# Kernel optimization log

Measured on AMD Instinct MI355X. Metric: run time of the kernel, lower is better.

Reference implementation:

```python
import jax, jax.numpy as jnp
import numpy as np

N_HEAD = 16

def setup_inputs() -> dict:
    key = jax.random.key(0)
    k1, k2, k3, k4, k5 = jax.random.split(key, 5)
    B, S, D = 2, 2048, 1024
    return {
        "hidden_states": jax.random.normal(k1, (B, S, D), jnp.float32),
        "w_attn": jax.random.normal(k2, (D, 3 * D), jnp.float32) * 0.02,
        "b_attn": jax.random.normal(k3, (3 * D,), jnp.float32) * 0.02,
        "w_proj": jax.random.normal(k4, (D, D), jnp.float32) * 0.02,
        "b_proj": jax.random.normal(k5, (D,), jnp.float32) * 0.02,
    }

def reference(hidden_states, w_attn, b_attn, w_proj, b_proj):
    B, S, D = hidden_states.shape
    H = N_HEAD
    Dh = D // H
    qkv = hidden_states @ w_attn + b_attn              # [B,S,3D]
    q, k, v = jnp.split(qkv, 3, axis=-1)
    def split_heads(x):
        return x.reshape(B, S, H, Dh).transpose(0, 2, 1, 3)  # [B,H,S,Dh]
    q, k, v = split_heads(q), split_heads(k), split_heads(v)
    # scale=True: divide by sqrt(head_dim) (v.size(-1))
    scores = jnp.einsum("bhqd,bhkd->bhqk", q, k) / jnp.sqrt(jnp.float32(Dh))
    attn = jax.nn.softmax(scores, axis=-1)             # [B,H,S,S]
    out = jnp.einsum("bhqk,bhkd->bhqd", attn, v)       # [B,H,S,Dh]
    out = out.transpose(0, 2, 1, 3).reshape(B, S, D)   # merge heads
    return out @ w_proj + b_proj
```

## Files before the change

kernel.cpp:

```cpp
#include <hip/hip_runtime.h>
#include <hip/hip_bf16.h>

typedef __attribute__((ext_vector_type(8))) short bf16x8;
typedef __attribute__((ext_vector_type(4))) float f32x4;
typedef __attribute__((ext_vector_type(16))) float f32x16;

#define LOG2E 1.4426950408889634f

__device__ inline unsigned short f2bf(float f) {
  union { float f; unsigned u; } x; x.f = f;
  unsigned u = x.u;
  unsigned r = u + 0x7FFFu + ((u >> 16) & 1u);
  return (unsigned short)(r >> 16);
}

__device__ inline unsigned cvtpk(float lo, float hi) {
  unsigned r;
  asm("v_cvt_pk_bf16_f32 %0, %1, %2" : "=v"(r) : "v"(lo), "v"(hi));
  return r;
}

__device__ inline void gload16(const unsigned short* g, unsigned short* l) {
  __builtin_amdgcn_global_load_lds(
      (const __attribute__((address_space(1))) unsigned int*)g,
      (__attribute__((address_space(3))) unsigned int*)l, 16, 0, 0);
}

template <int J>
__device__ inline bf16x8 pack_pfrag(f32x16 p) {
  int X, Y, Z, W;
  asm("v_cvt_pk_bf16_f32 %0, %1, %2" : "=v"(X) : "v"(p[J + 0]), "v"(p[J + 1]));
  asm("v_cvt_pk_bf16_f32 %0, %1, %2" : "=v"(Y) : "v"(p[J + 2]), "v"(p[J + 3]));
  asm("v_cvt_pk_bf16_f32 %0, %1, %2" : "=v"(Z) : "v"(p[J + 4]), "v"(p[J + 5]));
  asm("v_cvt_pk_bf16_f32 %0, %1, %2" : "=v"(W) : "v"(p[J + 6]), "v"(p[J + 7]));
  asm("v_permlane32_swap_b32 %0, %1" : "+v"(X), "+v"(Z));
  asm("v_permlane32_swap_b32 %0, %1" : "+v"(Y), "+v"(W));
  union { int w[4]; bf16x8 v; } u;
  u.w[0] = X; u.w[1] = Y; u.w[2] = Z; u.w[3] = W;
  return u.v;
}

__global__ __launch_bounds__(256) void cvt_bf16(const float* __restrict__ X,
                                                unsigned short* __restrict__ Y, int n4) {
  int i = blockIdx.x * blockDim.x + threadIdx.x;
  int stride = gridDim.x * blockDim.x;
  for (; i < n4; i += stride) {
    float4 v = reinterpret_cast<const float4*>(X)[i];
    ushort4 o;
    o.x = f2bf(v.x); o.y = f2bf(v.y); o.z = f2bf(v.z); o.w = f2bf(v.w);
    reinterpret_cast<ushort4*>(Y)[i] = o;
  }
}

__global__ __launch_bounds__(256) void transpose_cvt(const float* __restrict__ W,
                                                     unsigned short* __restrict__ WT,
                                                     int K, int N) {
  __shared__ unsigned short Tl[64][72];
  const int t = threadIdx.x;
  const int n0 = blockIdx.x * 64, k0 = blockIdx.y * 64;
#pragma unroll
  for (int i = 0; i < 4; ++i) {
    int idx = t + i * 256;
    int r = idx >> 4, c4 = (idx & 15) << 2;
    float4 v = *reinterpret_cast<const float4*>(&W[(size_t)(k0 + r) * N + n0 + c4]);
    Tl[c4 + 0][r] = f2bf(v.x);
    Tl[c4 + 1][r] = f2bf(v.y);
    Tl[c4 + 2][r] = f2bf(v.z);
    Tl[c4 + 3][r] = f2bf(v.w);
  }
  __syncthreads();
#pragma unroll
  for (int i = 0; i < 2; ++i) {
    int idx = t + i * 256;
    int rr = idx >> 3, cc = (idx & 7) << 3;
    *reinterpret_cast<int4*>(&WT[(size_t)(n0 + rr) * K + k0 + cc]) =
        *reinterpret_cast<const int4*>(&Tl[rr][cc]);
  }
}

#define GST(bs, kt)                                                             \
  {                                                                             \
    const unsigned short* Ap = Ab + (kt) * 32;                                  \
    const unsigned short* Bp = Bb + (kt) * 32;                                  \
    _Pragma("unroll") for (int i = 0; i < 2; ++i) {                             \
      int row = i * 64 + wid * 16 + s_r;                                        \
      gload16(&Ap[(size_t)row * 1024 + s_c], &Al[bs][i * 2048 + wid * 512]);    \
      gload16(&Bp[(size_t)row * 1024 + s_c], &Bl[bs][i * 2048 + wid * 512]);    \
    }                                                                           \
  }

#define GBODY(br)                                                               \
  {                                                                             \
    bf16x8 af[4], bfv[4];                                                       \
    _Pragma("unroll") for (int mm = 0; mm < 4; ++mm) {                          \
      int row = wr + mm * 16 + lr;                                              \
      af[mm] = *reinterpret_cast<const bf16x8*>(                                \
          &Al[br][row * 32 + ((kq ^ (lr & 3)) << 3)]);                          \
    }                                                                           \
    _Pragma("unroll") for (int nn = 0; nn < 4; ++nn) {                          \
      int row = wc + nn * 16 + lr;                                              \
      bfv[nn] = *reinterpret_cast<const bf16x8*>(                               \
          &Bl[br][row * 32 + ((kq ^ (lr & 3)) << 3)]);                          \
    }                                                                           \
    _Pragma("unroll") for (int mm = 0; mm < 4; ++mm)                            \
      _Pragma("unroll") for (int nn = 0; nn < 4; ++nn)                          \
        acc[mm][nn] =                                                           \
            __builtin_amdgcn_mfma_f32_16x16x32_bf16(af[mm], bfv[nn],            \
                                                    acc[mm][nn], 0, 0, 0);      \
  }

#define VMC4 asm volatile("s_waitcnt vmcnt(4)" ::: "memory");
#define VMC0 asm volatile("s_waitcnt vmcnt(0)" ::: "memory");
#define BAR __builtin_amdgcn_s_barrier();

__global__ __launch_bounds__(256) void gemm_qkv_b(
    const unsigned short* __restrict__ A, const unsigned short* __restrict__ Bt,
    const float* __restrict__ bias,
    unsigned short* __restrict__ qw, unsigned short* __restrict__ kw,
    unsigned short* __restrict__ vtg) {
  __shared__ unsigned short Al[3][4096];
  __shared__ unsigned short Bl[3][4096];
  const int t = threadIdx.x, lane = t & 63, wid = t >> 6;
  const int wr = (wid >> 1) * 64, wc = (wid & 1) * 64;
  const int orig = blockIdx.x + 24 * blockIdx.y;
  const int nid = (orig & 7) * 96 + (orig >> 3);
  const int row0 = (nid / 24) * 128, col0 = (nid % 24) * 128;
  const int lr = lane & 15, kq = lane >> 4;
  const int s_r = lane >> 2;
  const int s_c = ((lane & 3) ^ (s_r & 3)) * 8;
  const unsigned short* Ab = A + (size_t)row0 * 1024;
  const unsigned short* Bb = Bt + (size_t)col0 * 1024;
  f32x4 acc[4][4] = {};

  GST(0, 0) GST(1, 1)
  VMC4 BAR
  for (int tt = 0; tt < 30; tt += 3) {
    GST(2, tt + 2) GBODY(0) VMC4 BAR
    GST(0, tt + 3) GBODY(1) VMC4 BAR
    GST(1, tt + 4) GBODY(2) VMC4 BAR
  }
  GBODY(0) VMC0 BAR
  GBODY(1)

  const int rbase = (lane >> 4) * 4;
#pragma unroll
  for (int mm = 0; mm < 4; ++mm) {
#pragma unroll
    for (int nn = 0; nn < 4; ++nn) {
      int c = col0 + wc + nn * 16 + lr;
      int which = c >> 10;
      int d = c & 1023;
      int h = d >> 6, dh = d & 63;
      float bv = bias[c];
      int m0 = row0 + wr + mm * 16 + rbase;
      int b = m0 >> 11, s0 = m0 & 2047;
      if (which == 2) {
        int kt = s0 >> 6, key0 = s0 & 63;
        ushort4 pv;
        pv.x = f2bf(acc[mm][nn][0] + bv);
        pv.y = f2bf(acc[mm][nn][1] + bv);
        pv.z = f2bf(acc[mm][nn][2] + bv);
        pv.w = f2bf(acc[mm][nn][3] + bv);
        *reinterpret_cast<ushort4*>(
            &vtg[(((size_t)(b * 16 + h) * 32 + kt) * 64 + dh) * 64 + key0]) = pv;
      } else {
        unsigned short* dst = (which == 0) ? qw : kw;
#pragma unroll
        for (int r = 0; r < 4; ++r)
          dst[(((size_t)b * 16 + h) * 2048 + (s0 + r)) * 64 + dh] = f2bf(acc[mm][nn][r] + bv);
      }
    }
  }
}

__global__ __launch_bounds__(256) void gemm_proj_b(
    const unsigned short* __restrict__ A, const unsigned short* __restrict__ Bt,
    const float* __restrict__ bias, float* __restrict__ out) {
  const int N = 1024;
  __shared__ unsigned short Al[3][4096];
  __shared__ unsigned short Bl[3][4096];
  const int t = threadIdx.x, lane = t & 63, wid = t >> 6;
  const int wr = (wid >> 1) * 64, wc = (wid & 1) * 64;
  const int orig = blockIdx.x + 8 * blockIdx.y;
  const int nid = (orig & 7) * 32 + (orig >> 3);
  const int row0 = (nid >> 3) * 128, col0 = (nid & 7) * 128;
  const int lr = lane & 15, kq = lane >> 4;
  const int s_r = lane >> 2;
  const int s_c = ((lane & 3) ^ (s_r & 3)) * 8;
  const unsigned short* Ab = A + (size_t)row0 * 1024;
  const unsigned short* Bb = Bt + (size_t)col0 * 1024;
  f32x4 acc[4][4] = {};

  GST(0, 0) GST(1, 1)
  VMC4 BAR
  for (int tt = 0; tt < 30; tt += 3) {
    GST(2, tt + 2) GBODY(0) VMC4 BAR
    GST(0, tt + 3) GBODY(1) VMC4 BAR
    GST(1, tt + 4) GBODY(2) VMC4 BAR
  }
  GBODY(0) VMC0 BAR
  GBODY(1)

  const int rbase = (lane >> 4) * 4;
#pragma unroll
  for (int mm = 0; mm < 4; ++mm) {
#pragma unroll
    for (int nn = 0; nn < 4; ++nn) {
      int c = col0 + wc + nn * 16 + lr;
      float bv = bias[c];
#pragma unroll
      for (int r = 0; r < 4; ++r) {
        int m = row0 + wr + mm * 16 + rbase + r;
        out[(size_t)m * N + c] = acc[mm][nn][r] + bv;
      }
    }
  }
}

__global__ __launch_bounds__(512, 4) void attn_kernel(
    const unsigned short* __restrict__ qw, const unsigned short* __restrict__ kw,
    const unsigned short* __restrict__ vtg, unsigned short* __restrict__ ow) {
  __shared__ char smem[65536];
  unsigned short* KV = (unsigned short*)smem;
  unsigned short* Ol = (unsigned short*)smem;
  float* EX = (float*)(smem + 18432);
  const int t = threadIdx.x, lane = t & 63, wid = t >> 6;
  const int half = wid >> 2, wq = wid & 3;
  const int l31 = lane & 31, hi = lane >> 5;
  const int orig = blockIdx.x + 16 * blockIdx.y;
  const int nid = (orig & 7) * 64 + (orig >> 3);
  const int qt = nid & 15, bh = nid >> 4;
  const int b = bh >> 4, h = bh & 15;
  const unsigned short* Qg = qw + (size_t)bh * 2048 * 64;
  const unsigned short* Kg = kw + (size_t)bh * 2048 * 64;
  const unsigned short* Vg = vtg + (size_t)bh * 32 * 4096;
  const int q0 = qt * 128 + wq * 32;
  const float F = 0.125f * LOG2E;
  const float mF = 16.0f * F;

  union { short s[8]; bf16x8 v; } one_u;
#pragma unroll
  for (int i = 0; i < 8; ++i) one_u.s[i] = (short)0x3F80;
  const bf16x8 ones = one_u.v;

  bf16x8 qf[4];
#pragma unroll
  for (int kc = 0; kc < 4; ++kc)
    qf[kc] = *reinterpret_cast<const bf16x8*>(&Qg[(q0 + l31) * 64 + kc * 16 + hi * 8]);

  f32x16 oA = {0,0,0,0,0,0,0,0,0,0,0,0,0,0,0,0};
  f32x16 oB = {0,0,0,0,0,0,0,0,0,0,0,0,0,0,0,0};
  f32x16 lC = {0,0,0,0,0,0,0,0,0,0,0,0,0,0,0,0};

  const int srow_lo = lane >> 3;
  const int scg = (lane & 7) ^ srow_lo;

#define STAGE(buf, kt)                                                              \
  {                                                                                 \
    const unsigned short* Kt = Kg + (size_t)(kt) * 4096;                            \
    const unsigned short* Vs = Vg + (size_t)(kt) * 4096;                            \
    unsigned short* Kl = KV + half * 16384 + (buf) * 8192;                          \
    unsigned short* Vl = Kl + 4096;                                                 \
    _Pragma("unroll") for (int i = 0; i < 2; ++i) {                                 \
      int chunk = wq * 2 + i;                                                       \
      int row = chunk * 8 + srow_lo;                                                \
      gload16(&Kt[row * 64 + scg * 8], &Kl[chunk * 512]);                           \
      gload16(&Vs[row * 64 + scg * 8], &Vl[chunk * 512]);                           \
    }                                                                               \
  }

  const int kt0 = half * 16;
  STAGE(0, kt0)

  for (int it = 0; it < 16; ++it) {
    const int cur = it & 1;
    if (it + 1 < 16) {
      STAGE(cur ^ 1, kt0 + it + 1)
      asm volatile("s_waitcnt vmcnt(4)" ::: "memory");
    } else {
      asm volatile("s_waitcnt vmcnt(0)" ::: "memory");
    }
    __builtin_amdgcn_s_barrier();
    const unsigned short* Kl = KV + half * 16384 + cur * 8192;
    const unsigned short* Vl = Kl + 4096;

    f32x16 sA = {0,0,0,0,0,0,0,0,0,0,0,0,0,0,0,0};
    f32x16 sB = {0,0,0,0,0,0,0,0,0,0,0,0,0,0,0,0};
    __builtin_amdgcn_s_setprio(1);
#pragma unroll
    for (int kc = 0; kc < 4; ++kc) {
      bf16x8 k0f = *reinterpret_cast<const bf16x8*>(
          &Kl[l31 * 64 + (((kc * 2 + hi) ^ (l31 & 7)) << 3)]);
      bf16x8 k1f = *reinterpret_cast<const bf16x8*>(
          &Kl[(32 + l31) * 64 + (((kc * 2 + hi) ^ (l31 & 7)) << 3)]);
      sA = __builtin_amdgcn_mfma_f32_32x32x16_bf16(k0f, qf[kc], sA, 0, 0, 0);
      sB = __builtin_amdgcn_mfma_f32_32x32x16_bf16(k1f, qf[kc], sB, 0, 0, 0);
    }
    __builtin_amdgcn_s_setprio(0);

#pragma unroll
    for (int j = 0; j < 16; ++j) {
      sA[j] = exp2f(sA[j] * F - mF);
      sB[j] = exp2f(sB[j] * F - mF);
    }

    bf16x8 pf0 = pack_pfrag<0>(sA);
    bf16x8 pf1 = pack_pfrag<8>(sA);
    bf16x8 pf2 = pack_pfrag<0>(sB);
    bf16x8 pf3 = pack_pfrag<8>(sB);

    __builtin_amdgcn_s_setprio(1);
#pragma unroll
    for (int c = 0; c < 4; ++c) {
      bf16x8 pf = (c == 0) ? pf0 : (c == 1) ? pf1 : (c == 2) ? pf2 : pf3;
      int g = c * 2 + hi;
      bf16x8 v0f = *reinterpret_cast<const bf16x8*>(
          &Vl[l31 * 64 + ((g ^ (l31 & 7)) << 3)]);
      bf16x8 v1f = *reinterpret_cast<const bf16x8*>(
          &Vl[(32 + l31) * 64 + ((g ^ (l31 & 7)) << 3)]);
      oA = __builtin_amdgcn_mfma_f32_32x32x16_bf16(v0f, pf, oA, 0, 0, 0);
      oB = __builtin_amdgcn_mfma_f32_32x32x16_bf16(v1f, pf, oB, 0, 0, 0);
      lC = __builtin_amdgcn_mfma_f32_32x32x16_bf16(ones, pf, lC, 0, 0, 0);
    }
    __builtin_amdgcn_s_setprio(0);
    __builtin_amdgcn_s_barrier();
  }
#undef STAGE

  __syncthreads();
  if (half == 1) {
    float* e = EX + ((size_t)(wq * 64 + lane)) * 34;
#pragma unroll
    for (int j = 0; j < 16; ++j) { e[j] = oA[j]; e[16 + j] = oB[j]; }
    e[32] = lC[0];
  }
  __syncthreads();
  if (half == 0) {
    const float* e = EX + ((size_t)(wq * 64 + lane)) * 34;
    float linv = 1.0f / (lC[0] + e[32]);
    unsigned short* orow_l = Ol + (wq * 32 + l31) * 72;
#pragma unroll
    for (int g = 0; g < 4; ++g) {
      float a0 = (oA[4 * g + 0] + e[4 * g + 0]) * linv;
      float a1v = (oA[4 * g + 1] + e[4 * g + 1]) * linv;
      float a2v = (oA[4 * g + 2] + e[4 * g + 2]) * linv;
      float a3v = (oA[4 * g + 3] + e[4 * g + 3]) * linv;
      uint2 w0; w0.x = cvtpk(a0, a1v); w0.y = cvtpk(a2v, a3v);
      *reinterpret_cast<uint2*>(&orow_l[8 * g + 4 * hi]) = w0;
      float b0 = (oB[4 * g + 0] + e[16 + 4 * g + 0]) * linv;
      float b1v = (oB[4 * g + 1] + e[16 + 4 * g + 1]) * linv;
      float b2v = (oB[4 * g + 2] + e[16 + 4 * g + 2]) * linv;
      float b3v = (oB[4 * g + 3] + e[16 + 4 * g + 3]) * linv;
      uint2 w1; w1.x = cvtpk(b0, b1v); w1.y = cvtpk(b2v, b3v);
      *reinterpret_cast<uint2*>(&orow_l[32 + 8 * g + 4 * hi]) = w1;
    }
  }
  __syncthreads();
#pragma unroll
  for (int i = 0; i < 2; ++i) {
    int idx = t + i * 512;
    int q = idx >> 3, ch = idx & 7;
    int4 v = *reinterpret_cast<const int4*>(&Ol[q * 72 + ch * 8]);
    *reinterpret_cast<int4*>(
        &ow[(((size_t)b * 2048 + qt * 128 + q) * 16 + h) * 64 + ch * 8]) = v;
  }
}

extern "C" void kernel_launch(void* const* d_in, const int* in_sizes, int n_in,
                              void* d_out, int out_size, void* d_ws, size_t ws_size,
                              hipStream_t stream) {
  const float* hs = (const float*)d_in[0];
  const float* w_attn = (const float*)d_in[1];
  const float* b_attn = (const float*)d_in[2];
  const float* w_proj = (const float*)d_in[3];
  const float* b_proj = (const float*)d_in[4];
  float* out = (float*)d_out;

  const size_t HEAD = (size_t)2 * 16 * 2048 * 64;
  unsigned short* qw = (unsigned short*)d_ws;
  unsigned short* kw = qw + HEAD;
  unsigned short* vtg = kw + HEAD;
  unsigned short* hs_b = vtg + HEAD;
  unsigned short* ow = hs_b;
  unsigned short* wT = hs_b + HEAD;
  unsigned short* pT = wT + (size_t)3072 * 1024;

  cvt_bf16<<<2048, 256, 0, stream>>>(hs, hs_b, 1048576);
  transpose_cvt<<<dim3(48, 16), 256, 0, stream>>>(w_attn, wT, 1024, 3072);
  transpose_cvt<<<dim3(16, 16), 256, 0, stream>>>(w_proj, pT, 1024, 1024);

  gemm_qkv_b<<<dim3(24, 32), 256, 0, stream>>>(hs_b, wT, b_attn, qw, kw, vtg);
  attn_kernel<<<dim3(16, 32), 512, 0, stream>>>(qw, kw, vtg, ow);
  gemm_proj_b<<<dim3(8, 32), 256, 0, stream>>>(ow, pT, b_proj, out);
}
```

Baseline: 140.5 us.

## Replace QKV GEMM with 256x256-tile 8-wave ping-pong pipelined kernel

```diff
diff --git a/kernel.cpp b/kernel.cpp
--- a/kernel.cpp
+++ b/kernel.cpp
@@ -75,6 +75,136 @@
     int rr = idx >> 3, cc = (idx & 7) << 3;
     *reinterpret_cast<int4*>(&WT[(size_t)(n0 + rr) * K + k0 + cc]) =
         *reinterpret_cast<const int4*>(&Tl[rr][cc]);
+  }
+}
+
+__global__ __launch_bounds__(512, 2) void gemm_qkv_8p(
+    const unsigned short* __restrict__ A, const unsigned short* __restrict__ Bt,
+    const float* __restrict__ bias,
+    unsigned short* __restrict__ qw, unsigned short* __restrict__ kw,
+    unsigned short* __restrict__ vtg) {
+  __shared__ unsigned short Abuf[2][16384];
+  __shared__ unsigned short Bbuf[2][16384];
+  const int t = threadIdx.x, lane = t & 63, wid = t >> 6;
+  const int wm = wid >> 2, wn = wid & 3;
+  const int orig = blockIdx.x;
+  const int nid = (orig & 7) * 24 + (orig >> 3);
+  const int mt = nid / 12, nt = nid % 12;
+  const int row0 = mt * 256, col0 = nt * 256;
+  const int lr = lane & 15, kq = lane >> 4;
+  const int srow_lo = lane >> 3;
+  const int scg = (lane & 7) ^ srow_lo;
+  const unsigned short* Ab = A + (size_t)row0 * 1024;
+  const unsigned short* Bb = Bt + (size_t)col0 * 1024;
+  f32x4 acc[8][4] = {};
+
+#define SA8(bs, kt)                                                              \
+  {                                                                              \
+    const unsigned short* Ap = Ab + (kt) * 64;                                   \
+    _Pragma("unroll") for (int h = 0; h < 2; ++h)                                \
+    _Pragma("unroll") for (int i = 0; i < 2; ++i) {                              \
+      int rrel = h * 128 + (wid * 2 + i) * 8 + srow_lo;                          \
+      gload16(&Ap[(size_t)rrel * 1024 + scg * 8],                                \
+              &Abuf[bs][(h * 16 + wid * 2 + i) * 512]);                          \
+    }                                                                            \
+  }
+#define SB8(bs, kt)                                                              \
+  {                                                                              \
+    const unsigned short* Bp = Bb + (kt) * 64;                                   \
+    _Pragma("unroll") for (int h = 0; h < 2; ++h)                                \
+    _Pragma("unroll") for (int i = 0; i < 2; ++i) {                              \
+      int rrel = h * 128 + (wid * 2 + i) * 8 + srow_lo;                          \
+      gload16(&Bp[(size_t)rrel * 1024 + scg * 8],                                \
+              &Bbuf[bs][(h * 16 + wid * 2 + i) * 512]);                          \
+    }                                                                            \
+  }
+#define RDA(dst, mh)                                                             \
+  _Pragma("unroll") for (int m = 0; m < 4; ++m)                                  \
+  _Pragma("unroll") for (int ks = 0; ks < 2; ++ks) {                             \
+    int row = wm * 128 + (mh) * 64 + m * 16 + lr;                                \
+    dst[m][ks] = *reinterpret_cast<const bf16x8*>(                               \
+        &Ac[row * 64 + (((ks * 4 + kq) ^ (lr & 7)) << 3)]);                      \
+  }
+#define RDB(dst, nh)                                                             \
+  _Pragma("unroll") for (int n = 0; n < 2; ++n)                                  \
+  _Pragma("unroll") for (int ks = 0; ks < 2; ++ks) {                             \
+    int row = wn * 64 + (nh) * 32 + n * 16 + lr;                                 \
+    dst[n][ks] = *reinterpret_cast<const bf16x8*>(                               \
+        &Bc[row * 64 + (((ks * 4 + kq) ^ (lr & 7)) << 3)]);                      \
+  }
+#define QMM(mh, nh, afv, bfv)                                                    \
+  _Pragma("unroll") for (int m = 0; m < 4; ++m)                                  \
+  _Pragma("unroll") for (int n = 0; n < 2; ++n)                                  \
+  _Pragma("unroll") for (int ks = 0; ks < 2; ++ks)                               \
+    acc[(mh) * 4 + m][(nh) * 2 + n] = __builtin_amdgcn_mfma_f32_16x16x32_bf16(   \
+        afv[m][ks], bfv[n][ks], acc[(mh) * 4 + m][(nh) * 2 + n], 0, 0, 0);
+#define BAR8 __builtin_amdgcn_s_barrier();
+
+  SA8(0, 0) SB8(0, 0)
+  asm volatile("s_waitcnt vmcnt(0)" ::: "memory");
+  BAR8
+  __builtin_amdgcn_sched_barrier(0);
+
+  for (int kt = 0; kt < 16; ++kt) {
+    const int buf = kt & 1;
+    const unsigned short* Ac = Abuf[buf];
+    const unsigned short* Bc = Bbuf[buf];
+    bf16x8 af0[4][2], af1[4][2], bf0[2][2], bf1[2][2];
+    RDA(af0, 0) RDB(bf0, 0)
+    if (kt < 15) SA8(buf ^ 1, kt + 1)
+    BAR8
+    __builtin_amdgcn_s_setprio(1); QMM(0, 0, af0, bf0) __builtin_amdgcn_s_setprio(0);
+    BAR8
+    RDA(af1, 1)
+    if (kt < 15) SB8(buf ^ 1, kt + 1)
+    BAR8
+    __builtin_amdgcn_s_setprio(1); QMM(1, 0, af1, bf0) __builtin_amdgcn_s_setprio(0);
+    BAR8
+    RDB(bf1, 1)
+    BAR8
+    __builtin_amdgcn_s_setprio(1); QMM(0, 1, af0, bf1) __builtin_amdgcn_s_setprio(0);
+    BAR8
+    if (kt < 15) { asm volatile("s_waitcnt vmcnt(0)" ::: "memory"); }
+    BAR8
+    __builtin_amdgcn_s_setprio(1); QMM(1, 1, af1, bf1) __builtin_amdgcn_s_setprio(0);
+    BAR8
+    __builtin_amdgcn_sched_barrier(0);
+  }
+#undef SA8
+#undef SB8
+#undef RDA
+#undef RDB
+#undef QMM
+#undef BAR8
+
+  const int rbase = (lane >> 4) * 4;
+#pragma unroll
+  for (int mm = 0; mm < 8; ++mm) {
+#pragma unroll
+    for (int nn = 0; nn < 4; ++nn) {
+      int c = col0 + wn * 64 + nn * 16 + lr;
+      int which = c >> 10;
+      int d = c & 1023;
+      int h = d >> 6, dh = d & 63;
+      float bv = bias[c];
+      int m0 = row0 + wm * 128 + mm * 16 + rbase;
+      int b = m0 >> 11, s0 = m0 & 2047;
+      if (which == 2) {
+        int kt = s0 >> 6, key0 = s0 & 63;
+        ushort4 pv;
+        pv.x = f2bf(acc[mm][nn][0] + bv);
+        pv.y = f2bf(acc[mm][nn][1] + bv);
+        pv.z = f2bf(acc[mm][nn][2] + bv);
+        pv.w = f2bf(acc[mm][nn][3] + bv);
+        *reinterpret_cast<ushort4*>(
+            &vtg[(((size_t)(b * 16 + h) * 32 + kt) * 64 + dh) * 64 + key0]) = pv;
+      } else {
+        unsigned short* dst = (which == 0) ? qw : kw;
+#pragma unroll
+        for (int r = 0; r < 4; ++r)
+          dst[(((size_t)b * 16 + h) * 2048 + (s0 + r)) * 64 + dh] = f2bf(acc[mm][nn][r] + bv);
+      }
+    }
   }
 }
 
@@ -112,66 +242,6 @@
 #define VMC4 asm volatile("s_waitcnt vmcnt(4)" ::: "memory");
 #define VMC0 asm volatile("s_waitcnt vmcnt(0)" ::: "memory");
 #define BAR __builtin_amdgcn_s_barrier();
-
-__global__ __launch_bounds__(256) void gemm_qkv_b(
-    const unsigned short* __restrict__ A, const unsigned short* __restrict__ Bt,
-    const float* __restrict__ bias,
-    unsigned short* __restrict__ qw, unsigned short* __restrict__ kw,
-    unsigned short* __restrict__ vtg) {
-  __shared__ unsigned short Al[3][4096];
-  __shared__ unsigned short Bl[3][4096];
-  const int t = threadIdx.x, lane = t & 63, wid = t >> 6;
-  const int wr = (wid >> 1) * 64, wc = (wid & 1) * 64;
-  const int orig = blockIdx.x + 24 * blockIdx.y;
-  const int nid = (orig & 7) * 96 + (orig >> 3);
-  const int row0 = (nid / 24) * 128, col0 = (nid % 24) * 128;
-  const int lr = lane & 15, kq = lane >> 4;
-  const int s_r = lane >> 2;
-  const int s_c = ((lane & 3) ^ (s_r & 3)) * 8;
-  const unsigned short* Ab = A + (size_t)row0 * 1024;
-  const unsigned short* Bb = Bt + (size_t)col0 * 1024;
-  f32x4 acc[4][4] = {};
-
-  GST(0, 0) GST(1, 1)
-  VMC4 BAR
-  for (int tt = 0; tt < 30; tt += 3) {
-    GST(2, tt + 2) GBODY(0) VMC4 BAR
-    GST(0, tt + 3) GBODY(1) VMC4 BAR
-    GST(1, tt + 4) GBODY(2) VMC4 BAR
-  }
-  GBODY(0) VMC0 BAR
-  GBODY(1)
-
-  const int rbase = (lane >> 4) * 4;
-#pragma unroll
-  for (int mm = 0; mm < 4; ++mm) {
-#pragma unroll
-    for (int nn = 0; nn < 4; ++nn) {
-      int c = col0 + wc + nn * 16 + lr;
-      int which = c >> 10;
-      int d = c & 1023;
-      int h = d >> 6, dh = d & 63;
-      float bv = bias[c];
-      int m0 = row0 + wr + mm * 16 + rbase;
-      int b = m0 >> 11, s0 = m0 & 2047;
-      if (which == 2) {
-        int kt = s0 >> 6, key0 = s0 & 63;
-        ushort4 pv;
-        pv.x = f2bf(acc[mm][nn][0] + bv);
-        pv.y = f2bf(acc[mm][nn][1] + bv);
-        pv.z = f2bf(acc[mm][nn][2] + bv);
-        pv.w = f2bf(acc[mm][nn][3] + bv);
-        *reinterpret_cast<ushort4*>(
-            &vtg[(((size_t)(b * 16 + h) * 32 + kt) * 64 + dh) * 64 + key0]) = pv;
-      } else {
-        unsigned short* dst = (which == 0) ? qw : kw;
-#pragma unroll
-        for (int r = 0; r < 4; ++r)
-          dst[(((size_t)b * 16 + h) * 2048 + (s0 + r)) * 64 + dh] = f2bf(acc[mm][nn][r] + bv);
-      }
-    }
-  }
-}
 
 __global__ __launch_bounds__(256) void gemm_proj_b(
     const unsigned short* __restrict__ A, const unsigned short* __restrict__ Bt,
@@ -389,7 +459,7 @@
   transpose_cvt<<<dim3(48, 16), 256, 0, stream>>>(w_attn, wT, 1024, 3072);
   transpose_cvt<<<dim3(16, 16), 256, 0, stream>>>(w_proj, pT, 1024, 1024);
 
-  gemm_qkv_b<<<dim3(24, 32), 256, 0, stream>>>(hs_b, wT, b_attn, qw, kw, vtg);
+  gemm_qkv_8p<<<dim3(192), 512, 0, stream>>>(hs_b, wT, b_attn, qw, kw, vtg);
   attn_kernel<<<dim3(16, 32), 512, 0, stream>>>(qw, kw, vtg, ow);
   gemm_proj_b<<<dim3(8, 32), 256, 0, stream>>>(ow, pT, b_proj, out);
 }
```

Result: faster. 131.7 us (-6.3%).
